# Kernel tuning notes

Measured on AMD Instinct MI355X. Metric: run time of the kernel, lower is better.

## Reference

```python
import jax, jax.numpy as jnp
import numpy as np

EPS = 1e-6  # annotated-transformer LayerNorm eps


def setup_inputs() -> dict:
    key = jax.random.key(0)
    ks = jax.random.split(key, 6)
    B, S, D, F, G_dom = 32, 512, 1024, 2048, 4
    x = jax.random.normal(ks[0], (B, S, D), dtype=jnp.float32)
    # disjoint partition of the batch into 4 equal domain groups (like the
    # per-domain LongTensor index lists in the torch forward)
    perm = jax.random.permutation(ks[1], B).astype(jnp.int32)
    idx = perm.reshape(G_dom, B // G_dom)  # [4, 8]
    s1 = 1.0 / np.sqrt(D)
    s2 = 1.0 / np.sqrt(F)
    W1 = jax.random.normal(ks[2], (G_dom, D, F), dtype=jnp.float32) * s1
    B1 = jnp.zeros((G_dom, F), dtype=jnp.float32)
    W2 = jax.random.normal(ks[3], (G_dom, F, D), dtype=jnp.float32) * s2
    B2 = jnp.zeros((G_dom, D), dtype=jnp.float32)
    G = jnp.ones((G_dom, D), dtype=jnp.float32)
    Bn = jnp.zeros((G_dom, D), dtype=jnp.float32)
    return {"x": x, "idx": idx, "W1": W1, "B1": B1, "W2": W2, "B2": B2,
            "G": G, "Bn": Bn}


def _layer_norm(x, g, b):
    # matches torch: a_2 * (x - mean) / (std + eps) + b_2, std unbiased (ddof=1)
    mu = jnp.mean(x, axis=-1, keepdims=True)
    sd = jnp.std(x, axis=-1, keepdims=True, ddof=1)
    return g * (x - mu) / (sd + EPS) + b


def reference(x, idx, W1, B1, W2, B2, G, Bn):
    # gather per-domain token groups: [n_dom, per_dom, S, D]
    xg = x[idx]
    # SublayerConnection (eval mode, dropout off): x + adapter(norm(x))
    h = _layer_norm(xg, G[:, None, None, :], Bn[:, None, None, :])
    h = jax.nn.relu(jnp.einsum('gbsd,gdf->gbsf', h, W1) + B1[:, None, None, :])
    a = jnp.einsum('gbsf,gfd->gbsd', h, W2) + B2[:, None, None, :]
    out_g = xg + a
    # scatter combine (index_copy): indices are a disjoint partition
    S_, D_ = x.shape[1], x.shape[2]
    out = jnp.zeros_like(x).at[idx.reshape(-1)].set(out_g.reshape(-1, S_, D_))
    return out
```

## Files before the change

### kernel.cpp

```cpp
#include <hip/hip_runtime.h>
#include <hip/hip_bf16.h>


#define S_DIM 512
#define D_DIM 1024
#define F_DIM 2048
#define MPG   4096

typedef __attribute__((ext_vector_type(8))) short  short8;
typedef __attribute__((ext_vector_type(4))) float  f32x4;

__device__ __forceinline__ void gll16(const void* g, void* l) {
  __builtin_amdgcn_global_load_lds((__attribute__((address_space(1))) void*)g,
                                   (__attribute__((address_space(3))) void*)l,
                                   16, 0, 0);
}
#define VMC4()  asm volatile("s_waitcnt vmcnt(4)" ::: "memory")
#define LGKM0() asm volatile("s_waitcnt lgkmcnt(0)" ::: "memory")
#define SB()    __builtin_amdgcn_sched_barrier(0)
#define BAR()   __builtin_amdgcn_s_barrier()

__global__ __launch_bounds__(256) void transpose_cast_kernel(
    const float* __restrict__ W1, const float* __restrict__ W2,
    __hip_bfloat16* __restrict__ W1t, __hip_bfloat16* __restrict__ W2t)
{
  __shared__ float tl[32][33];
  const int bid = blockIdx.x;
  const float* src; __hip_bfloat16* dst;
  int R, C, tr, tc;
  if (bid < 8192) {
    const int g = bid >> 11, t = bid & 2047;
    R = 1024; C = 2048; tr = t >> 6; tc = t & 63;
    src = W1 + (size_t)g * R * C;
    dst = W1t + (size_t)g * R * C;
  } else {
    const int b2 = bid - 8192;
    const int g = b2 >> 11, t = b2 & 2047;
    R = 2048; C = 1024; tr = t >> 5; tc = t & 31;
    src = W2 + (size_t)g * R * C;
    dst = W2t + (size_t)g * R * C;
  }
  const int tx = threadIdx.x & 31, ty = threadIdx.x >> 5;
  const int r0 = tr * 32, c0 = tc * 32;
#pragma unroll
  for (int i = 0; i < 4; ++i)
    tl[ty + 8 * i][tx] = src[(size_t)(r0 + ty + 8 * i) * C + (c0 + tx)];
  __syncthreads();
#pragma unroll
  for (int i = 0; i < 4; ++i)
    dst[(size_t)(c0 + ty + 8 * i) * R + (r0 + tx)] = __float2bfloat16(tl[tx][ty + 8 * i]);
}

__global__ __launch_bounds__(256) void ln_gather_kernel(
    const float* __restrict__ x, const int* __restrict__ idx,
    const float* __restrict__ G, const float* __restrict__ Bn,
    __hip_bfloat16* __restrict__ Xn)
{
  const int wid  = (blockIdx.x * 256 + threadIdx.x) >> 6;
  const int lane = threadIdx.x & 63;
  const int g = wid >> 12;
  const int r = wid & 4095;
  const int j = r >> 9;
  const int tok = r & 511;
  const int b = idx[g * 8 + j];

  const float* src = x + ((size_t)b * S_DIM + tok) * D_DIM + lane * 16;
  float4 vq[4];
#pragma unroll
  for (int i = 0; i < 4; ++i) vq[i] = ((const float4*)src)[i];
  const float* va = (const float*)vq;

  float s = 0.f, s2 = 0.f;
#pragma unroll
  for (int i = 0; i < 16; ++i) { s += va[i]; s2 += va[i] * va[i]; }
#pragma unroll
  for (int o = 32; o > 0; o >>= 1) { s += __shfl_xor(s, o); s2 += __shfl_xor(s2, o); }

  const float mu  = s * (1.0f / 1024.0f);
  float var = fmaxf(s2 * (1.0f / 1024.0f) - mu * mu, 0.0f) * (1024.0f / 1023.0f);
  const float rs  = 1.0f / (sqrtf(var) + 1e-6f);

  float4 gq[4], bq[4];
  const float* gp = G  + (size_t)g * D_DIM + lane * 16;
  const float* bp = Bn + (size_t)g * D_DIM + lane * 16;
#pragma unroll
  for (int i = 0; i < 4; ++i) { gq[i] = ((const float4*)gp)[i]; bq[i] = ((const float4*)bp)[i]; }
  const float* ga = (const float*)gq;
  const float* be = (const float*)bq;

  __align__(16) __hip_bfloat16 ob[16];
#pragma unroll
  for (int i = 0; i < 16; ++i)
    ob[i] = __float2bfloat16(ga[i] * (va[i] - mu) * rs + be[i]);

  __hip_bfloat16* dst = Xn + ((size_t)g * MPG + r) * D_DIM + lane * 16;
  ((uint4*)dst)[0] = *(const uint4*)&ob[0];
  ((uint4*)dst)[1] = *(const uint4*)&ob[8];
}

template <bool SECOND>
__global__ __launch_bounds__(512, 2) void gemm_kernel(
    const __hip_bfloat16* __restrict__ A,
    const __hip_bfloat16* __restrict__ Bw,
    const float* __restrict__ bias,
    const float* __restrict__ xres,
    const int* __restrict__ idx,
    __hip_bfloat16* __restrict__ obf,
    float* __restrict__ of32,
    const int N, const int K, const int NT)
{
  extern __shared__ char lds[];
  const int ntile = N >> 8;
  const int nwg = gridDim.x;
  const int bid0 = blockIdx.x;
  const int bid = (bid0 & 7) * (nwg >> 3) + (bid0 >> 3);
  const int mt = bid / ntile, nt = bid % ntile;
  const int g  = mt >> 4;
  const int tid = threadIdx.x;
  const int w = tid >> 6, lane = tid & 63;
  const int wm = w >> 2, wn = w & 3;

  const __hip_bfloat16* Ab = A + (size_t)mt * 256 * K;
  const __hip_bfloat16* Bb = Bw + ((size_t)g * N + (size_t)nt * 256) * K;

  const int sp   = (lane & 7) ^ ((lane >> 3) & 7);
  const int srow = 2 * (lane >> 3) + (sp >> 2);
  const int skof = (sp & 3) * 8;
  const __hip_bfloat16* Ag0 = Ab + (size_t)(w * 32 + srow) * K + skof;
  const __hip_bfloat16* Ag1 = Ag0 + (size_t)16 * K;
  const __hip_bfloat16* Bg0 = Bb + (size_t)(w * 32 + srow) * K + skof;
  const __hip_bfloat16* Bg1 = Bg0 + (size_t)16 * K;

  const int l15 = lane & 15, sl = lane >> 4;
  const int slot_phys = (((l15 & 1) << 2) + sl) ^ ((l15 >> 1) & 7);
  const int lane_c = ((l15 >> 1) << 7) + (slot_phys << 4);

  f32x4 acc[8][4] = {};
  short8 frA[4], frB[4];

#define STAGE(BUFX, MAT, KH, TN) {                                          \
    const int koff = (TN) * 64 + (KH) * 32;                                 \
    char* d = lds + (BUFX) + ((KH) * 2 + (MAT)) * 16384 + w * 2048;         \
    if (MAT) { gll16(Bg0 + koff, d); gll16(Bg1 + koff, d + 1024); }         \
    else     { gll16(Ag0 + koff, d); gll16(Ag1 + koff, d + 1024); } }

#define RDA(BUFX, KH, MH) {                                                 \
    const char* base_ = lds + (BUFX) + (KH) * 32768 + wm * 8192 +           \
                        (MH) * 4096 + lane_c;                               \
    _Pragma("unroll") for (int mm = 0; mm < 4; ++mm)                        \
      frA[mm] = *(const short8*)(base_ + mm * 1024); }

#define RDB(BUFX, KH) {                                                     \
    const char* base_ = lds + (BUFX) + 16384 + (KH) * 32768 + wn * 4096 +   \
                        lane_c;                                             \
    _Pragma("unroll") for (int n = 0; n < 4; ++n)                           \
      frB[n] = *(const short8*)(base_ + n * 1024); }

#define MF(MH) {                                                            \
    __builtin_amdgcn_s_setprio(1);                                          \
    _Pragma("unroll") for (int mm = 0; mm < 4; ++mm)                        \
      _Pragma("unroll") for (int n = 0; n < 4; ++n)                         \
        acc[(MH) * 4 + mm][n] = __builtin_amdgcn_mfma_f32_16x16x32_bf16(    \
            frA[mm], frB[n], acc[(MH) * 4 + mm][n], 0, 0, 0);               \
    __builtin_amdgcn_s_setprio(0); }

  STAGE(0, 0, 0, 0); STAGE(0, 1, 0, 0); STAGE(0, 0, 1, 0); STAGE(0, 1, 1, 0);
  VMC4();
  BAR();

  for (int t = 0; t < NT; ++t) {
    const int bufb = (t & 1) << 16;
    const int bufx = bufb ^ 65536;
    const int tn = (t + 1 == NT) ? 0 : t + 1;
    RDA(bufb, 0, 0); RDB(bufb, 0);
    STAGE(bufx, 0, 0, tn);
    SB(); BAR(); LGKM0(); SB();
    MF(0);
    BAR();
    RDA(bufb, 0, 1);
    STAGE(bufx, 1, 0, tn);
    VMC4();
    SB(); BAR(); LGKM0(); SB();
    MF(1);
    BAR();
    RDA(bufb, 1, 0); RDB(bufb, 1);
    STAGE(bufx, 0, 1, tn);
    SB(); BAR(); LGKM0(); SB();
    MF(0);
    BAR();
    RDA(bufb, 1, 1);
    STAGE(bufx, 1, 1, tn);
    VMC4();
    SB(); BAR(); LGKM0(); SB();
    MF(1);
    BAR();
  }
#undef STAGE
#undef RDA
#undef RDB
#undef MF

  const int cc  = lane & 15;
  const int cr4 = (lane >> 4) * 4;

  float bv[4];
#pragma unroll
  for (int n = 0; n < 4; ++n)
    bv[n] = bias[(size_t)g * N + nt * 256 + wn * 64 + n * 16 + cc];

  if constexpr (!SECOND) {
#pragma unroll
    for (int m = 0; m < 8; ++m) {
      const int grow0 = mt * 256 + wm * 128 + m * 16 + cr4;
#pragma unroll
      for (int n = 0; n < 4; ++n) {
        const int gcol = nt * 256 + wn * 64 + n * 16 + cc;
#pragma unroll
        for (int i = 0; i < 4; ++i) {
          const float v = fmaxf(acc[m][n][i] + bv[n], 0.0f);
          obf[(size_t)(grow0 + i) * N + gcol] = __float2bfloat16(v);
        }
      }
    }
  } else {
    const int rbase = (mt & 15) * 256;
    const int b = idx[g * 8 + (rbase >> 9)];
    const size_t ob = (size_t)b * S_DIM * D_DIM;
#pragma unroll
    for (int m = 0; m < 8; ++m) {
      const int rloc = rbase + wm * 128 + m * 16 + cr4;
#pragma unroll
      for (int n = 0; n < 4; ++n) {
        const int gcol = nt * 256 + wn * 64 + n * 16 + cc;
#pragma unroll
        for (int i = 0; i < 4; ++i) {
          const int tok = (rloc + i) & 511;
          const size_t off = ob + (size_t)tok * D_DIM + gcol;
          of32[off] = acc[m][n][i] + bv[n] + xres[off];
        }
      }
    }
  }
}

extern "C" void kernel_launch(void* const* d_in, const int* in_sizes, int n_in,
                              void* d_out, int out_size, void* d_ws, size_t ws_size,
                              hipStream_t stream) {
  const float* x  = (const float*)d_in[0];
  const int*   idx = (const int*)d_in[1];
  const float* W1 = (const float*)d_in[2];
  const float* B1 = (const float*)d_in[3];
  const float* W2 = (const float*)d_in[4];
  const float* B2 = (const float*)d_in[5];
  const float* G  = (const float*)d_in[6];
  const float* Bn = (const float*)d_in[7];
  float* out = (float*)d_out;

  char* ws = (char*)d_ws;
  __hip_bfloat16* Xn  = (__hip_bfloat16*)(ws);
  __hip_bfloat16* W1t = (__hip_bfloat16*)(ws + 33554432);
  __hip_bfloat16* W2t = (__hip_bfloat16*)(ws + 50331648);
  __hip_bfloat16* H1  = (__hip_bfloat16*)(ws + 67108864);

  (void)hipFuncSetAttribute((const void*)gemm_kernel<false>,
                            hipFuncAttributeMaxDynamicSharedMemorySize, 131072);
  (void)hipFuncSetAttribute((const void*)gemm_kernel<true>,
                            hipFuncAttributeMaxDynamicSharedMemorySize, 131072);

  transpose_cast_kernel<<<dim3(16384), dim3(256), 0, stream>>>(W1, W2, W1t, W2t);
  ln_gather_kernel<<<dim3(4096), dim3(256), 0, stream>>>(x, idx, G, Bn, Xn);
  gemm_kernel<false><<<dim3(512), dim3(512), 131072, stream>>>(
      Xn, W1t, B1, nullptr, nullptr, H1, nullptr, F_DIM, D_DIM, 16);
  gemm_kernel<true><<<dim3(256), dim3(512), 131072, stream>>>(
      H1, W2t, B2, x, idx, nullptr, out, D_DIM, F_DIM, 32);
}
```

Measured before the change: 189.1 us.

## Restructure GEMM main-loop barriers and stage epilogue through LDS for vectorized stores

The main loop is reordered so each half-iteration waits on vmcnt and a barrier before reading LDS, and the explicit lgkmcnt waits and sched barriers are dropped. The final iteration no longer issues redundant prefetch loads. The epilogue now stages accumulator tiles per wave through LDS so each lane writes 16-byte vectorized bf16 or float4 stores, and reads the residual with vector loads, instead of scattered scalar stores. This adds LDS traffic and relies on the compiler to insert the correct LDS waits, which risks ordering hazards now that the explicit waits are gone.

Measured after the change: 183.9 us. 2.8% less time.

```diff
diff --git a/kernel.cpp b/kernel.cpp
--- a/kernel.cpp
+++ b/kernel.cpp
@@ -16,8 +16,6 @@
                                    16, 0, 0);
 }
 #define VMC4()  asm volatile("s_waitcnt vmcnt(4)" ::: "memory")
-#define LGKM0() asm volatile("s_waitcnt lgkmcnt(0)" ::: "memory")
-#define SB()    __builtin_amdgcn_sched_barrier(0)
 #define BAR()   __builtin_amdgcn_s_barrier()
 
 __global__ __launch_bounds__(256) void transpose_cast_kernel(
@@ -165,35 +163,30 @@
     __builtin_amdgcn_s_setprio(0); }
 
   STAGE(0, 0, 0, 0); STAGE(0, 1, 0, 0); STAGE(0, 0, 1, 0); STAGE(0, 1, 1, 0);
-  VMC4();
-  BAR();
 
   for (int t = 0; t < NT; ++t) {
     const int bufb = (t & 1) << 16;
     const int bufx = bufb ^ 65536;
-    const int tn = (t + 1 == NT) ? 0 : t + 1;
-    RDA(bufb, 0, 0); RDB(bufb, 0);
-    STAGE(bufx, 0, 0, tn);
-    SB(); BAR(); LGKM0(); SB();
+    const int more = (t + 1 < NT);
+    const int tn = more ? t + 1 : 0;
+    VMC4();
+    BAR();
+    RDB(bufb, 0); RDA(bufb, 0, 0);
+    if (more) STAGE(bufx, 0, 0, tn);
     MF(0);
     BAR();
     RDA(bufb, 0, 1);
-    STAGE(bufx, 1, 0, tn);
+    if (more) STAGE(bufx, 1, 0, tn);
+    MF(1);
     VMC4();
-    SB(); BAR(); LGKM0(); SB();
+    BAR();
+    RDB(bufb, 1); RDA(bufb, 1, 0);
+    if (more) STAGE(bufx, 0, 1, tn);
+    MF(0);
+    BAR();
+    RDA(bufb, 1, 1);
+    if (more) STAGE(bufx, 1, 1, tn);
     MF(1);
-    BAR();
-    RDA(bufb, 1, 0); RDB(bufb, 1);
-    STAGE(bufx, 0, 1, tn);
-    SB(); BAR(); LGKM0(); SB();
-    MF(0);
-    BAR();
-    RDA(bufb, 1, 1);
-    STAGE(bufx, 1, 1, tn);
-    VMC4();
-    SB(); BAR(); LGKM0(); SB();
-    MF(1);
-    BAR();
   }
 #undef STAGE
 #undef RDA
@@ -208,18 +201,31 @@
   for (int n = 0; n < 4; ++n)
     bv[n] = bias[(size_t)g * N + nt * 256 + wn * 64 + n * 16 + cc];
 
+  float* wsl = (float*)(lds + w * 4352);
+  const int rr  = lane >> 3;
+  const int c8  = (lane & 7) * 8;
+  const int gcol0 = nt * 256 + wn * 64 + c8;
+
   if constexpr (!SECOND) {
 #pragma unroll
-    for (int m = 0; m < 8; ++m) {
-      const int grow0 = mt * 256 + wm * 128 + m * 16 + cr4;
-#pragma unroll
-      for (int n = 0; n < 4; ++n) {
-        const int gcol = nt * 256 + wn * 64 + n * 16 + cc;
-#pragma unroll
-        for (int i = 0; i < 4; ++i) {
-          const float v = fmaxf(acc[m][n][i] + bv[n], 0.0f);
-          obf[(size_t)(grow0 + i) * N + gcol] = __float2bfloat16(v);
-        }
+    for (int p = 0; p < 8; ++p) {
+#pragma unroll
+      for (int n = 0; n < 4; ++n)
+#pragma unroll
+        for (int i = 0; i < 4; ++i)
+          wsl[(cr4 + i) * 68 + n * 16 + cc] = fmaxf(acc[p][n][i] + bv[n], 0.0f);
+      const int grow0 = mt * 256 + wm * 128 + p * 16;
+#pragma unroll
+      for (int it = 0; it < 2; ++it) {
+        const int r = it * 8 + rr;
+        float4 v0 = *(const float4*)&wsl[r * 68 + c8];
+        float4 v1 = *(const float4*)&wsl[r * 68 + c8 + 4];
+        __align__(16) __hip_bfloat16 ob[8];
+        ob[0] = __float2bfloat16(v0.x); ob[1] = __float2bfloat16(v0.y);
+        ob[2] = __float2bfloat16(v0.z); ob[3] = __float2bfloat16(v0.w);
+        ob[4] = __float2bfloat16(v1.x); ob[5] = __float2bfloat16(v1.y);
+        ob[6] = __float2bfloat16(v1.z); ob[7] = __float2bfloat16(v1.w);
+        *(uint4*)&obf[(size_t)(grow0 + r) * N + gcol0] = *(const uint4*)ob;
       }
     }
   } else {
@@ -227,17 +233,26 @@
     const int b = idx[g * 8 + (rbase >> 9)];
     const size_t ob = (size_t)b * S_DIM * D_DIM;
 #pragma unroll
-    for (int m = 0; m < 8; ++m) {
-      const int rloc = rbase + wm * 128 + m * 16 + cr4;
-#pragma unroll
-      for (int n = 0; n < 4; ++n) {
-        const int gcol = nt * 256 + wn * 64 + n * 16 + cc;
-#pragma unroll
-        for (int i = 0; i < 4; ++i) {
-          const int tok = (rloc + i) & 511;
-          const size_t off = ob + (size_t)tok * D_DIM + gcol;
-          of32[off] = acc[m][n][i] + bv[n] + xres[off];
-        }
+    for (int p = 0; p < 8; ++p) {
+#pragma unroll
+      for (int n = 0; n < 4; ++n)
+#pragma unroll
+        for (int i = 0; i < 4; ++i)
+          wsl[(cr4 + i) * 68 + n * 16 + cc] = acc[p][n][i] + bv[n];
+      const int rloc0 = rbase + wm * 128 + p * 16;
+#pragma unroll
+      for (int it = 0; it < 2; ++it) {
+        const int r = it * 8 + rr;
+        const int tok = (rloc0 + r) & 511;
+        const size_t off = ob + (size_t)tok * D_DIM + gcol0;
+        float4 v0 = *(const float4*)&wsl[r * 68 + c8];
+        float4 v1 = *(const float4*)&wsl[r * 68 + c8 + 4];
+        float4 x0 = *(const float4*)&xres[off];
+        float4 x1 = *(const float4*)&xres[off + 4];
+        v0.x += x0.x; v0.y += x0.y; v0.z += x0.z; v0.w += x0.w;
+        v1.x += x1.x; v1.y += x1.y; v1.z += x1.z; v1.w += x1.w;
+        *(float4*)&of32[off]     = v0;
+        *(float4*)&of32[off + 4] = v1;
       }
     }
   }
```
